# Kernel optimization log

Measured on AMD Instinct MI355X. Metric: run time of the kernel, lower is better.

Reference implementation:

```python
import jax, jax.numpy as jnp
import numpy as np

DIM = 512
NUM_HEADS = 16
WS = 8  # window_size
N = WS * WS
B = 1024


def get_relative_index(h, w):
    coords_h = np.arange(h)[:, None].repeat(w, axis=1)
    coords_w = np.arange(w)[None, :].repeat(h, axis=0)
    coords = np.stack([coords_h, coords_w], axis=-1).reshape(-1, 2)  # [N,2]
    rel = coords[:, None, :] - coords[None, :, :]
    rel = rel + np.array([h - 1, w - 1])
    rel[:, :, 0] *= 2 * w - 1
    return rel.sum(-1).astype(np.int32)  # [N,N]


def setup_inputs() -> dict:
    key = jax.random.key(0)
    ks = jax.random.split(key, 6)
    table_size = (2 * WS - 1) * (2 * WS - 1)  # 225
    return {
        "x": jax.random.normal(ks[0], (B, N, DIM), dtype=jnp.float32),
        "qkv_weight": jax.random.normal(ks[1], (3 * DIM, DIM), dtype=jnp.float32) * 0.02,
        "qkv_bias": jax.random.normal(ks[2], (3 * DIM,), dtype=jnp.float32) * 0.02,
        "proj_weight": jax.random.normal(ks[3], (DIM, DIM), dtype=jnp.float32) * 0.02,
        "proj_bias": jax.random.normal(ks[4], (DIM,), dtype=jnp.float32) * 0.02,
        "relative_table": jax.random.normal(ks[5], (table_size, 2 * NUM_HEADS), dtype=jnp.float32) * 0.02,
        "relative_index": jnp.asarray(get_relative_index(WS, WS)),
    }


def reference(x, qkv_weight, qkv_bias, proj_weight, proj_bias, relative_table, relative_index):
    B_, n, C = x.shape
    H = NUM_HEADS
    hd = C // H
    scale = hd ** -0.5
    # qkv projection: [B,N,3C] -> [3,B,H,N,hd]
    qkv = (x @ qkv_weight.T + qkv_bias).reshape(B_, n, 3, H, hd).transpose(2, 0, 3, 1, 4)
    q, k, v = qkv[0], qkv[1], qkv[2]
    attn = jnp.einsum("bhnd,bhmd->bhnm", q * scale, k)  # [B,H,N,N]
    # learned relative-position bias + post-softmax scale
    params = relative_table[relative_index.reshape(-1)].reshape(n, n, 2 * H)
    params = params.transpose(2, 0, 1)  # [2H,N,N]
    rel_bias, rel_scale = params[:H], params[H:]
    attn = jax.nn.softmax(attn + rel_bias[None], axis=-1)
    attn = attn * rel_scale[None]
    out = jnp.einsum("bhnm,bhmd->bhnd", attn, v)
    out = out.transpose(0, 2, 1, 3).reshape(B_, n, C)
    return out @ proj_weight.T + proj_bias
```

## Files before the change

kernel.cpp:

```cpp
#include <hip/hip_runtime.h>

typedef unsigned short u16;
typedef unsigned int   u32;
typedef __attribute__((ext_vector_type(8))) short bf16x8;
typedef __attribute__((ext_vector_type(4))) float f32x4;

#define SCALE 0.17677669529663687f

__device__ __forceinline__ u16 f2bf(float f){
  u32 x = __float_as_uint(f);
  x += 0x7fffu + ((x >> 16) & 1u);
  return (u16)(x >> 16);
}
__device__ __forceinline__ float bf2f(u16 u){
  return __uint_as_float(((u32)u) << 16);
}


__global__ void prep_kernel(const float* __restrict__ qkvw, const float* __restrict__ projw,
                            const float* __restrict__ table, const int* __restrict__ relidx,
                            u16* __restrict__ qkvw_b, u16* __restrict__ projw_b,
                            u16* __restrict__ biasT, u16* __restrict__ scaleT){
  int i = blockIdx.x * 256 + threadIdx.x;
  if (i < 786432) {
    qkvw_b[i] = f2bf(qkvw[i]);
  } else if (i < 1048576) {
    int j = i - 786432; projw_b[j] = f2bf(projw[j]);
  } else if (i < 1114112) {
    int j = i - 1048576; int h = j >> 12, rc = j & 4095;
    int idx = relidx[rc];
    biasT [h*4096 + rc] = f2bf(table[idx*32 + h]);
    scaleT[h*4096 + rc] = f2bf(table[idx*32 + 16 + h]);
  }
}

__global__ void xconv_kernel(const float* __restrict__ x, u16* __restrict__ xb){
  size_t i = (size_t)blockIdx.x * 256 + threadIdx.x;
  const float4* xp = (const float4*)x;
  float4 a = xp[2*i], b = xp[2*i+1];
  union { u16 u[8]; uint4 v; } o;
  o.u[0]=f2bf(a.x); o.u[1]=f2bf(a.y); o.u[2]=f2bf(a.z); o.u[3]=f2bf(a.w);
  o.u[4]=f2bf(b.x); o.u[5]=f2bf(b.y); o.u[6]=f2bf(b.z); o.u[7]=f2bf(b.w);
  *(uint4*)(xb + 8*i) = o.v;
}

template<int EPI>
__global__ __launch_bounds__(512, 4) void gemm_kernel(
    const u16* __restrict__ A, const u16* __restrict__ W,
    const float* __restrict__ bias, void* __restrict__ outp, const int NT)
{
  __shared__ u16 lds[3][12288];
  const int tid = threadIdx.x, lane = tid & 63;
  const int wid = tid >> 6, wave_base = tid & ~63;

  const int cpx = gridDim.x >> 3;
  const int bid = (blockIdx.x & 7) * cpx + (blockIdx.x >> 3);
  const int mt = bid / NT, nt = bid % NT;
  const size_t m0 = (size_t)mt * 128;
  const int n0 = nt * 256;
  const int wm = wid >> 2, wn = wid & 3;

  const f32x4 z = {0.f, 0.f, 0.f, 0.f};
  f32x4 acc[4][4];
#pragma unroll
  for (int i = 0; i < 4; i++)
#pragma unroll
    for (int j = 0; j < 4; j++) acc[i][j] = z;

  auto stage = [&](int ch){
    const int slot = ch % 3;
    const int kb = ch * 32;
    {
      const int row = tid >> 2, sl = tid & 3;
      const int lsl = sl ^ ((row >> 1) & 3);
      const u16* ga = A + (m0 + row)*512 + kb + lsl*8;
      u16* la = &lds[slot][(size_t)wave_base*8];
      __builtin_amdgcn_global_load_lds((const __attribute__((address_space(1))) u32*)ga,
                                       (__attribute__((address_space(3))) u32*)la, 16, 0, 0);
    }
#pragma unroll
    for (int c = 0; c < 2; ++c){
      const int t = c*512 + tid;
      const int col = t >> 2, sl = t & 3;
      const int lsl = sl ^ ((col >> 1) & 3);
      const u16* gb = W + (size_t)(n0 + col)*512 + kb + lsl*8;
      u16* lb = &lds[slot][4096 + (size_t)(c*512 + wave_base)*8];
      __builtin_amdgcn_global_load_lds((const __attribute__((address_space(1))) u32*)gb,
                                       (__attribute__((address_space(3))) u32*)lb, 16, 0, 0);
    }
  };

  stage(0);
  stage(1);
  asm volatile("s_waitcnt vmcnt(3)" ::: "memory");
  __builtin_amdgcn_s_barrier();

  const int lq = lane & 15, lk = lane >> 4;
#pragma unroll
  for (int ch = 0; ch < 16; ++ch){
    const int slot = ch % 3;
    if (ch + 2 < 16) stage(ch + 2);
    const u16* As = &lds[slot][0];
    const u16* Bs = &lds[slot][4096];
    bf16x8 af[4], bfr[4];
#pragma unroll
    for (int i = 0; i < 4; ++i){
      const int row = wm*64 + i*16 + lq;
      af[i]  = *(const bf16x8*)&As[row*32 + (lk ^ ((row >> 1) & 3))*8];
      const int col = wn*64 + i*16 + lq;
      bfr[i] = *(const bf16x8*)&Bs[col*32 + (lk ^ ((col >> 1) & 3))*8];
    }
    asm volatile("s_waitcnt lgkmcnt(0)" ::: "memory");
    __builtin_amdgcn_sched_barrier(0);
    __builtin_amdgcn_s_setprio(1);
#pragma unroll
    for (int i = 0; i < 4; ++i)
#pragma unroll
      for (int j = 0; j < 4; ++j)
        acc[i][j] = __builtin_amdgcn_mfma_f32_16x16x32_bf16(af[i], bfr[j], acc[i][j], 0, 0, 0);
    __builtin_amdgcn_s_setprio(0);
    if (ch <= 13)      { asm volatile("s_waitcnt vmcnt(3)" ::: "memory"); }
    else if (ch == 14) { asm volatile("s_waitcnt vmcnt(0)" ::: "memory"); }
    if (ch < 15) __builtin_amdgcn_s_barrier();
  }

  const int lr = (lane >> 4) << 2;
  const int lc = lane & 15;
  if (EPI == 0){
    u16* o = (u16*)outp;
    float bv[4], sc[4];
#pragma unroll
    for (int nf = 0; nf < 4; ++nf){
      const int col = n0 + wn*64 + nf*16 + lc;
      bv[nf] = bias[col];
      sc[nf] = (col < 512) ? SCALE : 1.f;
    }
#pragma unroll
    for (int mf = 0; mf < 4; ++mf){
#pragma unroll
      for (int r = 0; r < 4; ++r){
        const size_t row = m0 + wm*64 + mf*16 + lr + r;
#pragma unroll
        for (int nf = 0; nf < 4; ++nf){
          const int col = n0 + wn*64 + nf*16 + lc;
          o[row*1536 + col] = f2bf((acc[mf][nf][r] + bv[nf]) * sc[nf]);
        }
      }
    }
  } else {
    float* o = (float*)outp;
    float bv[4];
#pragma unroll
    for (int nf = 0; nf < 4; ++nf)
      bv[nf] = bias[n0 + wn*64 + nf*16 + lc];
#pragma unroll
    for (int mf = 0; mf < 4; ++mf){
#pragma unroll
      for (int r = 0; r < 4; ++r){
        const size_t row = m0 + wm*64 + mf*16 + lr + r;
#pragma unroll
        for (int nf = 0; nf < 4; ++nf){
          const int col = n0 + wn*64 + nf*16 + lc;
          o[row*512 + col] = acc[mf][nf][r] + bv[nf];
        }
      }
    }
  }
}

__global__ __launch_bounds__(256) void attn_kernel(
    const u16* __restrict__ qkv, const u16* __restrict__ biasT,
    const u16* __restrict__ scaleT, u16* __restrict__ attn_out)
{
  __shared__ u16 qs[64*40];
  __shared__ u16 ks[64*40];
  __shared__ u16 vs[64*40];
  __shared__ u16 Ps[64*72];
  const int tid = threadIdx.x, lane = tid & 63, wid = tid >> 6;
  const int bh = blockIdx.x, b = bh >> 4, h = bh & 15;
  const u16* base = qkv + (size_t)b * 64 * 1536 + h * 32;
  {
    const int row = tid >> 2, seg = (tid & 3) * 8;
    const size_t ro = (size_t)row * 1536 + seg;
    *(uint4*)&qs[row*40 + seg] = *(const uint4*)(base + ro);
    *(uint4*)&ks[row*40 + seg] = *(const uint4*)(base + ro + 512);
    *(uint4*)&vs[row*40 + seg] = *(const uint4*)(base + ro + 1024);
  }
  __syncthreads();

  const int wr0 = wid * 16;
  const int lg = lane >> 4, lc = lane & 15;
  const f32x4 z = {0.f, 0.f, 0.f, 0.f};

  bf16x8 qf = *(const bf16x8*)&qs[(wr0 + lc)*40 + lg*8];
  f32x4 s[4];
#pragma unroll
  for (int ct = 0; ct < 4; ++ct){
    bf16x8 kf = *(const bf16x8*)&ks[(ct*16 + lc)*40 + lg*8];
    s[ct] = __builtin_amdgcn_mfma_f32_16x16x32_bf16(qf, kf, z, 0, 0, 0);
  }

  const u16* bT = biasT + h*4096;
  const u16* sT = scaleT + h*4096;
#pragma unroll
  for (int r = 0; r < 4; ++r){
    const int row = wr0 + lg*4 + r;
    float vals[4]; float mx = -1e30f;
#pragma unroll
    for (int ct = 0; ct < 4; ++ct){
      vals[ct] = s[ct][r] + bf2f(bT[row*64 + ct*16 + lc]);
      mx = fmaxf(mx, vals[ct]);
    }
    mx = fmaxf(mx, __shfl_xor(mx, 1));
    mx = fmaxf(mx, __shfl_xor(mx, 2));
    mx = fmaxf(mx, __shfl_xor(mx, 4));
    mx = fmaxf(mx, __shfl_xor(mx, 8));
    float sm = 0.f;
#pragma unroll
    for (int ct = 0; ct < 4; ++ct){ vals[ct] = __expf(vals[ct] - mx); sm += vals[ct]; }
    sm += __shfl_xor(sm, 1);
    sm += __shfl_xor(sm, 2);
    sm += __shfl_xor(sm, 4);
    sm += __shfl_xor(sm, 8);
    const float inv = 1.f / sm;
#pragma unroll
    for (int ct = 0; ct < 4; ++ct){
      const int col = ct*16 + lc;
      Ps[row*72 + col] = f2bf(vals[ct] * inv * bf2f(sT[row*64 + col]));
    }
  }
  __syncthreads();

  f32x4 o[2] = {z, z};
#pragma unroll
  for (int kc = 0; kc < 2; ++kc){
    bf16x8 pf = *(const bf16x8*)&Ps[(wr0 + lc)*72 + kc*32 + lg*8];
#pragma unroll
    for (int c2 = 0; c2 < 2; ++c2){
      union { u16 u[8]; bf16x8 v; } vf;
#pragma unroll
      for (int e = 0; e < 8; ++e)
        vf.u[e] = vs[(kc*32 + lg*8 + e)*40 + c2*16 + lc];
      o[c2] = __builtin_amdgcn_mfma_f32_16x16x32_bf16(pf, vf.v, o[c2], 0, 0, 0);
    }
  }

#pragma unroll
  for (int c2 = 0; c2 < 2; ++c2){
#pragma unroll
    for (int r = 0; r < 4; ++r){
      const int n = wr0 + lg*4 + r;
      attn_out[((size_t)b*64 + n)*512 + h*32 + c2*16 + lc] = f2bf(o[c2][r]);
    }
  }
}

extern "C" void kernel_launch(void* const* d_in, const int* in_sizes, int n_in,
                              void* d_out, int out_size, void* d_ws, size_t ws_size,
                              hipStream_t stream)
{
  const float* x      = (const float*)d_in[0];
  const float* qkvw   = (const float*)d_in[1];
  const float* qkvb   = (const float*)d_in[2];
  const float* projw  = (const float*)d_in[3];
  const float* projb  = (const float*)d_in[4];
  const float* table  = (const float*)d_in[5];
  const int*   relidx = (const int*)d_in[6];
  char* ws = (char*)d_ws;

  u16* qkvw_b = (u16*)(ws + 0);
  u16* projw_b= (u16*)(ws + 1572864);
  u16* biasT  = (u16*)(ws + 2097152);
  u16* scaleT = (u16*)(ws + 2228224);
  u16* qkvws  = (u16*)(ws + 2359296);
  u16* xb     = (u16*)(ws + 203685888);
  u16* attn_o = xb;

  if (ws_size < 270794752ull) return;

  prep_kernel<<<dim3(4352), dim3(256), 0, stream>>>(qkvw, projw, table, relidx,
                                                    qkvw_b, projw_b, biasT, scaleT);
  xconv_kernel<<<dim3(16384), dim3(256), 0, stream>>>(x, xb);
  gemm_kernel<0><<<dim3(3072), dim3(512), 0, stream>>>(xb, qkvw_b, qkvb, (void*)qkvws, 6);
  attn_kernel<<<dim3(16384), dim3(256), 0, stream>>>(qkvws, biasT, scaleT, attn_o);
  gemm_kernel<1><<<dim3(1024), dim3(512), 0, stream>>>(attn_o, projw_b, projb, d_out, 2);
}
```

Before: 296.4 us.

## Enlarge GEMM tile to 256x256 with K=64 double-buffered 8-phase pipeline

Both GEMMs now use 256x256 output tiles per block instead of 128x256, with each wave computing 128x64, and the grid sizes are halved to match. K is staged in chunks of 64, with two LDS buffers and an XOR swizzle over 8 slots. The main loop is split into eight phases per iteration, each phase interleaving half-tile global-to-LDS loads with MFMA work and reusing the B fragments across the two M halves. The aim is higher arithmetic intensity and fewer redundant global loads per FLOP. In exchange, register and LDS pressure rise (launch bounds drop to 2 blocks per CU), the block count falls, and many more barriers are added.

```diff
diff --git a/kernel.cpp b/kernel.cpp
--- a/kernel.cpp
+++ b/kernel.cpp
@@ -45,84 +45,109 @@
 }
 
 template<int EPI>
-__global__ __launch_bounds__(512, 4) void gemm_kernel(
+__global__ __launch_bounds__(512, 2) void gemm_kernel(
     const u16* __restrict__ A, const u16* __restrict__ W,
     const float* __restrict__ bias, void* __restrict__ outp, const int NT)
 {
-  __shared__ u16 lds[3][12288];
+  __shared__ u16 lds[2][32768];
   const int tid = threadIdx.x, lane = tid & 63;
   const int wid = tid >> 6, wave_base = tid & ~63;
 
   const int cpx = gridDim.x >> 3;
   const int bid = (blockIdx.x & 7) * cpx + (blockIdx.x >> 3);
   const int mt = bid / NT, nt = bid % NT;
-  const size_t m0 = (size_t)mt * 128;
+  const size_t m0 = (size_t)mt * 256;
   const int n0 = nt * 256;
   const int wm = wid >> 2, wn = wid & 3;
+  const int lq = lane & 15, lk = lane >> 4;
 
   const f32x4 z = {0.f, 0.f, 0.f, 0.f};
-  f32x4 acc[4][4];
-#pragma unroll
-  for (int i = 0; i < 4; i++)
+  f32x4 acc[8][4];
+#pragma unroll
+  for (int i = 0; i < 8; i++)
 #pragma unroll
     for (int j = 0; j < 4; j++) acc[i][j] = z;
 
-  auto stage = [&](int ch){
-    const int slot = ch % 3;
-    const int kb = ch * 32;
-    {
-      const int row = tid >> 2, sl = tid & 3;
-      const int lsl = sl ^ ((row >> 1) & 3);
-      const u16* ga = A + (m0 + row)*512 + kb + lsl*8;
-      u16* la = &lds[slot][(size_t)wave_base*8];
-      __builtin_amdgcn_global_load_lds((const __attribute__((address_space(1))) u32*)ga,
-                                       (__attribute__((address_space(3))) u32*)la, 16, 0, 0);
-    }
+  auto stage_half = [&](int t, int half){
+    const int buf = t & 1;
+    const int kb = t * 64;
+    const bool isB = half >= 2;
+    const int h01 = half & 1;
+    const u16* src = isB ? W : A;
+    const size_t r0 = isB ? (size_t)n0 : m0;
+    const int ldsoff = (isB ? 16384 : 0) + h01 * 8192;
 #pragma unroll
     for (int c = 0; c < 2; ++c){
-      const int t = c*512 + tid;
-      const int col = t >> 2, sl = t & 3;
-      const int lsl = sl ^ ((col >> 1) & 3);
-      const u16* gb = W + (size_t)(n0 + col)*512 + kb + lsl*8;
-      u16* lb = &lds[slot][4096 + (size_t)(c*512 + wave_base)*8];
-      __builtin_amdgcn_global_load_lds((const __attribute__((address_space(1))) u32*)gb,
-                                       (__attribute__((address_space(3))) u32*)lb, 16, 0, 0);
+      const int u = c*512 + tid;
+      const int tr = h01*128 + (u >> 3);
+      const int lsl = (u & 7) ^ (tr & 7);
+      const u16* g = src + (r0 + tr)*512 + kb + lsl*8;
+      u16* l = &lds[buf][ldsoff + (size_t)(c*512 + wave_base)*8];
+      __builtin_amdgcn_global_load_lds((const __attribute__((address_space(1))) u32*)g,
+                                       (__attribute__((address_space(3))) u32*)l, 16, 0, 0);
     }
   };
 
-  stage(0);
-  stage(1);
-  asm volatile("s_waitcnt vmcnt(3)" ::: "memory");
+  bf16x8 bfr[4];
+
+#define PHASE(BUF, MH, KH, READB, STAGE_STMT) do {                            \
+    bf16x8 af[4];                                                             \
+    _Pragma("unroll")                                                         \
+    for (int i_ = 0; i_ < 4; ++i_){                                           \
+      const int row_ = wm*128 + (MH)*64 + i_*16 + lq;                         \
+      af[i_] = *(const bf16x8*)&lds[BUF][row_*64 + (((KH)*4+lk)^(lq&7))*8];   \
+    }                                                                         \
+    if (READB){                                                               \
+      _Pragma("unroll")                                                       \
+      for (int j_ = 0; j_ < 4; ++j_){                                         \
+        const int col_ = wn*64 + j_*16 + lq;                                  \
+        bfr[j_] = *(const bf16x8*)&lds[BUF][16384 + col_*64 + (((KH)*4+lk)^(lq&7))*8]; \
+      }                                                                       \
+    }                                                                         \
+    STAGE_STMT;                                                               \
+    __builtin_amdgcn_s_barrier();                                             \
+    asm volatile("s_waitcnt lgkmcnt(0)" ::: "memory");                        \
+    __builtin_amdgcn_sched_barrier(0);                                        \
+    __builtin_amdgcn_s_setprio(1);                                            \
+    _Pragma("unroll")                                                         \
+    for (int i_ = 0; i_ < 4; ++i_)                                            \
+      _Pragma("unroll")                                                       \
+      for (int j_ = 0; j_ < 4; ++j_)                                          \
+        acc[(MH)*4+i_][j_] = __builtin_amdgcn_mfma_f32_16x16x32_bf16(         \
+            af[i_], bfr[j_], acc[(MH)*4+i_][j_], 0, 0, 0);                    \
+    __builtin_amdgcn_s_setprio(0);                                            \
+  } while(0)
+
+  stage_half(0, 0); stage_half(0, 1); stage_half(0, 2); stage_half(0, 3);
+  stage_half(1, 2);
+  asm volatile("s_waitcnt vmcnt(2)" ::: "memory");
   __builtin_amdgcn_s_barrier();
 
-  const int lq = lane & 15, lk = lane >> 4;
-#pragma unroll
-  for (int ch = 0; ch < 16; ++ch){
-    const int slot = ch % 3;
-    if (ch + 2 < 16) stage(ch + 2);
-    const u16* As = &lds[slot][0];
-    const u16* Bs = &lds[slot][4096];
-    bf16x8 af[4], bfr[4];
-#pragma unroll
-    for (int i = 0; i < 4; ++i){
-      const int row = wm*64 + i*16 + lq;
-      af[i]  = *(const bf16x8*)&As[row*32 + (lk ^ ((row >> 1) & 3))*8];
-      const int col = wn*64 + i*16 + lq;
-      bfr[i] = *(const bf16x8*)&Bs[col*32 + (lk ^ ((col >> 1) & 3))*8];
-    }
-    asm volatile("s_waitcnt lgkmcnt(0)" ::: "memory");
-    __builtin_amdgcn_sched_barrier(0);
-    __builtin_amdgcn_s_setprio(1);
-#pragma unroll
-    for (int i = 0; i < 4; ++i)
-#pragma unroll
-      for (int j = 0; j < 4; ++j)
-        acc[i][j] = __builtin_amdgcn_mfma_f32_16x16x32_bf16(af[i], bfr[j], acc[i][j], 0, 0, 0);
-    __builtin_amdgcn_s_setprio(0);
-    if (ch <= 13)      { asm volatile("s_waitcnt vmcnt(3)" ::: "memory"); }
-    else if (ch == 14) { asm volatile("s_waitcnt vmcnt(0)" ::: "memory"); }
-    if (ch < 15) __builtin_amdgcn_s_barrier();
-  }
+#pragma unroll
+  for (int it = 0; it < 4; ++it){
+    PHASE(0, 0, 0, true,  stage_half(2*it+1, 3));
+    __builtin_amdgcn_s_barrier();
+    PHASE(0, 1, 0, false, stage_half(2*it+1, 0));
+    __builtin_amdgcn_s_barrier();
+    PHASE(0, 0, 1, true,  stage_half(2*it+1, 1));
+    __builtin_amdgcn_s_barrier();
+    PHASE(0, 1, 1, false, if (it < 3) stage_half(2*it+2, 2));
+    if (it < 3) { asm volatile("s_waitcnt vmcnt(2)" ::: "memory"); }
+    else        { asm volatile("s_waitcnt vmcnt(0)" ::: "memory"); }
+    __builtin_amdgcn_s_barrier();
+    PHASE(1, 0, 0, true,  if (it < 3) stage_half(2*it+2, 3));
+    __builtin_amdgcn_s_barrier();
+    PHASE(1, 1, 0, false, if (it < 3) stage_half(2*it+2, 0));
+    __builtin_amdgcn_s_barrier();
+    PHASE(1, 0, 1, true,  if (it < 3) stage_half(2*it+2, 1));
+    __builtin_amdgcn_s_barrier();
+    PHASE(1, 1, 1, false, if (it < 3) stage_half(2*it+3, 2));
+    if (it < 3){
+      asm volatile("s_waitcnt vmcnt(2)" ::: "memory");
+      __builtin_amdgcn_s_barrier();
+    }
+  }
+#undef PHASE
 
   const int lr = (lane >> 4) << 2;
   const int lc = lane & 15;
@@ -136,10 +161,10 @@
       sc[nf] = (col < 512) ? SCALE : 1.f;
     }
 #pragma unroll
-    for (int mf = 0; mf < 4; ++mf){
+    for (int mf = 0; mf < 8; ++mf){
 #pragma unroll
       for (int r = 0; r < 4; ++r){
-        const size_t row = m0 + wm*64 + mf*16 + lr + r;
+        const size_t row = m0 + wm*128 + mf*16 + lr + r;
 #pragma unroll
         for (int nf = 0; nf < 4; ++nf){
           const int col = n0 + wn*64 + nf*16 + lc;
@@ -154,10 +179,10 @@
     for (int nf = 0; nf < 4; ++nf)
       bv[nf] = bias[n0 + wn*64 + nf*16 + lc];
 #pragma unroll
-    for (int mf = 0; mf < 4; ++mf){
+    for (int mf = 0; mf < 8; ++mf){
 #pragma unroll
       for (int r = 0; r < 4; ++r){
-        const size_t row = m0 + wm*64 + mf*16 + lr + r;
+        const size_t row = m0 + wm*128 + mf*16 + lr + r;
 #pragma unroll
         for (int nf = 0; nf < 4; ++nf){
           const int col = n0 + wn*64 + nf*16 + lc;
@@ -281,7 +306,7 @@
   prep_kernel<<<dim3(4352), dim3(256), 0, stream>>>(qkvw, projw, table, relidx,
                                                     qkvw_b, projw_b, biasT, scaleT);
   xconv_kernel<<<dim3(16384), dim3(256), 0, stream>>>(x, xb);
-  gemm_kernel<0><<<dim3(3072), dim3(512), 0, stream>>>(xb, qkvw_b, qkvb, (void*)qkvws, 6);
+  gemm_kernel<0><<<dim3(1536), dim3(512), 0, stream>>>(xb, qkvw_b, qkvb, (void*)qkvws, 6);
   attn_kernel<<<dim3(16384), dim3(256), 0, stream>>>(qkvws, biasT, scaleT, attn_o);
-  gemm_kernel<1><<<dim3(1024), dim3(512), 0, stream>>>(attn_o, projw_b, projb, d_out, 2);
-}
+  gemm_kernel<1><<<dim3(512), dim3(512), 0, stream>>>(attn_o, projw_b, projb, d_out, 2);
+}
```

Result: faster. 287.6 us (-3.0%).

## Fuse fp32-to-bf16 conversion of x into the QKV GEMM A-tile load

Applied to the files above, without the earlier changes.

Drops the separate x conversion kernel. The QKV GEMM now loads fp32 x directly into registers, converts to bf16 and writes the swizzled LDS tile, pipelined two chunks ahead alongside the async global_load_lds for weights. This avoids writing and re-reading a 64 MB bf16 copy of x plus one kernel launch. The cost is that x is re-read once for each of the 6 N-tiles, in fp32 at twice the bytes, and each iteration adds register pressure and conversion ALU work.

```diff
diff --git a/kernel.cpp b/kernel.cpp
--- a/kernel.cpp
+++ b/kernel.cpp
@@ -34,20 +34,9 @@
   }
 }
 
-__global__ void xconv_kernel(const float* __restrict__ x, u16* __restrict__ xb){
-  size_t i = (size_t)blockIdx.x * 256 + threadIdx.x;
-  const float4* xp = (const float4*)x;
-  float4 a = xp[2*i], b = xp[2*i+1];
-  union { u16 u[8]; uint4 v; } o;
-  o.u[0]=f2bf(a.x); o.u[1]=f2bf(a.y); o.u[2]=f2bf(a.z); o.u[3]=f2bf(a.w);
-  o.u[4]=f2bf(b.x); o.u[5]=f2bf(b.y); o.u[6]=f2bf(b.z); o.u[7]=f2bf(b.w);
-  *(uint4*)(xb + 8*i) = o.v;
-}
-
-template<int EPI>
-__global__ __launch_bounds__(512, 4) void gemm_kernel(
-    const u16* __restrict__ A, const u16* __restrict__ W,
-    const float* __restrict__ bias, void* __restrict__ outp, const int NT)
+__global__ __launch_bounds__(512, 4) void gemm_qkv_kernel(
+    const float* __restrict__ X, const u16* __restrict__ W,
+    const float* __restrict__ bias, u16* __restrict__ outp)
 {
   __shared__ u16 lds[3][12288];
   const int tid = threadIdx.x, lane = tid & 63;
@@ -55,7 +44,129 @@
 
   const int cpx = gridDim.x >> 3;
   const int bid = (blockIdx.x & 7) * cpx + (blockIdx.x >> 3);
-  const int mt = bid / NT, nt = bid % NT;
+  const int mt = bid / 6, nt = bid % 6;
+  const size_t m0 = (size_t)mt * 128;
+  const int n0 = nt * 256;
+  const int wm = wid >> 2, wn = wid & 3;
+
+  const f32x4 z = {0.f, 0.f, 0.f, 0.f};
+  f32x4 acc[4][4];
+#pragma unroll
+  for (int i = 0; i < 4; i++)
+#pragma unroll
+    for (int j = 0; j < 4; j++) acc[i][j] = z;
+
+  const int arow = tid >> 2, asl = tid & 3;
+  const float* ag = X + (m0 + arow)*512 + asl*8;
+  const int awoff = arow*32 + (asl ^ ((arow >> 1) & 3))*8;
+
+  float4 arg[2][2];
+
+  auto stageB = [&](int ch){
+    const int slot = ch % 3;
+    const int kb = ch * 32;
+#pragma unroll
+    for (int c = 0; c < 2; ++c){
+      const int t = c*512 + tid;
+      const int col = t >> 2, sl = t & 3;
+      const int lsl = sl ^ ((col >> 1) & 3);
+      const u16* gb = W + (size_t)(n0 + col)*512 + kb + lsl*8;
+      u16* lb = &lds[slot][4096 + (size_t)(c*512 + wave_base)*8];
+      __builtin_amdgcn_global_load_lds((const __attribute__((address_space(1))) u32*)gb,
+                                       (__attribute__((address_space(3))) u32*)lb, 16, 0, 0);
+    }
+  };
+  auto issueA = [&](int ch, int s){
+    arg[s][0] = *(const float4*)(ag + ch*32);
+    arg[s][1] = *(const float4*)(ag + ch*32 + 4);
+  };
+  auto writeA = [&](int ch, int s){
+    union { u16 u[8]; bf16x8 v; } o;
+    const float* f = (const float*)&arg[s][0];
+#pragma unroll
+    for (int e = 0; e < 8; ++e) o.u[e] = f2bf(f[e]);
+    *(bf16x8*)&lds[ch % 3][awoff] = o.v;
+  };
+
+  issueA(0, 0);
+  issueA(1, 1);
+  stageB(0); stageB(1);
+  asm volatile("s_waitcnt vmcnt(6)" ::: "memory");
+  writeA(0, 0);
+  asm volatile("s_waitcnt vmcnt(2)" ::: "memory");
+  asm volatile("s_waitcnt lgkmcnt(0)" ::: "memory");
+  __builtin_amdgcn_s_barrier();
+
+  const int lq = lane & 15, lk = lane >> 4;
+#pragma unroll
+  for (int ch = 0; ch < 16; ++ch){
+    const int slot = ch % 3;
+    if (ch + 2 < 16){ issueA(ch + 2, ch & 1); stageB(ch + 2); }
+    const u16* As = &lds[slot][0];
+    const u16* Bs = &lds[slot][4096];
+    bf16x8 af[4], bfr[4];
+#pragma unroll
+    for (int i = 0; i < 4; ++i){
+      const int row = wm*64 + i*16 + lq;
+      af[i]  = *(const bf16x8*)&As[row*32 + (lk ^ ((row >> 1) & 3))*8];
+      const int col = wn*64 + i*16 + lq;
+      bfr[i] = *(const bf16x8*)&Bs[col*32 + (lk ^ ((col >> 1) & 3))*8];
+    }
+    asm volatile("s_waitcnt lgkmcnt(0)" ::: "memory");
+    __builtin_amdgcn_sched_barrier(0);
+    __builtin_amdgcn_s_setprio(1);
+#pragma unroll
+    for (int i = 0; i < 4; ++i)
+#pragma unroll
+      for (int j = 0; j < 4; ++j)
+        acc[i][j] = __builtin_amdgcn_mfma_f32_16x16x32_bf16(af[i], bfr[j], acc[i][j], 0, 0, 0);
+    __builtin_amdgcn_s_setprio(0);
+    if (ch < 15){
+      if (ch + 2 < 16) { asm volatile("s_waitcnt vmcnt(6)" ::: "memory"); }
+      else             { asm volatile("s_waitcnt vmcnt(2)" ::: "memory"); }
+      writeA(ch + 1, (ch + 1) & 1);
+      if (ch + 2 < 16) { asm volatile("s_waitcnt vmcnt(4)" ::: "memory"); }
+      else             { asm volatile("s_waitcnt vmcnt(0)" ::: "memory"); }
+      asm volatile("s_waitcnt lgkmcnt(0)" ::: "memory");
+      __builtin_amdgcn_s_barrier();
+    }
+  }
+
+  const int lr = (lane >> 4) << 2;
+  const int lc = lane & 15;
+  u16* o = outp;
+  float bv[4], sc[4];
+#pragma unroll
+  for (int nf = 0; nf < 4; ++nf){
+    const int col = n0 + wn*64 + nf*16 + lc;
+    bv[nf] = bias[col];
+    sc[nf] = (col < 512) ? SCALE : 1.f;
+  }
+#pragma unroll
+  for (int mf = 0; mf < 4; ++mf){
+#pragma unroll
+    for (int r = 0; r < 4; ++r){
+      const size_t row = m0 + wm*64 + mf*16 + lr + r;
+#pragma unroll
+      for (int nf = 0; nf < 4; ++nf){
+        const int col = n0 + wn*64 + nf*16 + lc;
+        o[row*1536 + col] = f2bf((acc[mf][nf][r] + bv[nf]) * sc[nf]);
+      }
+    }
+  }
+}
+
+__global__ __launch_bounds__(512, 4) void gemm_proj_kernel(
+    const u16* __restrict__ A, const u16* __restrict__ W,
+    const float* __restrict__ bias, float* __restrict__ outp)
+{
+  __shared__ u16 lds[3][12288];
+  const int tid = threadIdx.x, lane = tid & 63;
+  const int wid = tid >> 6, wave_base = tid & ~63;
+
+  const int cpx = gridDim.x >> 3;
+  const int bid = (blockIdx.x & 7) * cpx + (blockIdx.x >> 3);
+  const int mt = bid >> 1, nt = bid & 1;
   const size_t m0 = (size_t)mt * 128;
   const int n0 = nt * 256;
   const int wm = wid >> 2, wn = wid & 3;
@@ -126,43 +237,19 @@
 
   const int lr = (lane >> 4) << 2;
   const int lc = lane & 15;
-  if (EPI == 0){
-    u16* o = (u16*)outp;
-    float bv[4], sc[4];
-#pragma unroll
-    for (int nf = 0; nf < 4; ++nf){
-      const int col = n0 + wn*64 + nf*16 + lc;
-      bv[nf] = bias[col];
-      sc[nf] = (col < 512) ? SCALE : 1.f;
-    }
-#pragma unroll
-    for (int mf = 0; mf < 4; ++mf){
-#pragma unroll
-      for (int r = 0; r < 4; ++r){
-        const size_t row = m0 + wm*64 + mf*16 + lr + r;
-#pragma unroll
-        for (int nf = 0; nf < 4; ++nf){
-          const int col = n0 + wn*64 + nf*16 + lc;
-          o[row*1536 + col] = f2bf((acc[mf][nf][r] + bv[nf]) * sc[nf]);
-        }
-      }
-    }
-  } else {
-    float* o = (float*)outp;
-    float bv[4];
-#pragma unroll
-    for (int nf = 0; nf < 4; ++nf)
-      bv[nf] = bias[n0 + wn*64 + nf*16 + lc];
-#pragma unroll
-    for (int mf = 0; mf < 4; ++mf){
-#pragma unroll
-      for (int r = 0; r < 4; ++r){
-        const size_t row = m0 + wm*64 + mf*16 + lr + r;
-#pragma unroll
-        for (int nf = 0; nf < 4; ++nf){
-          const int col = n0 + wn*64 + nf*16 + lc;
-          o[row*512 + col] = acc[mf][nf][r] + bv[nf];
-        }
+  float bv[4];
+#pragma unroll
+  for (int nf = 0; nf < 4; ++nf)
+    bv[nf] = bias[n0 + wn*64 + nf*16 + lc];
+#pragma unroll
+  for (int mf = 0; mf < 4; ++mf){
+#pragma unroll
+    for (int r = 0; r < 4; ++r){
+      const size_t row = m0 + wm*64 + mf*16 + lr + r;
+#pragma unroll
+      for (int nf = 0; nf < 4; ++nf){
+        const int col = n0 + wn*64 + nf*16 + lc;
+        outp[row*512 + col] = acc[mf][nf][r] + bv[nf];
       }
     }
   }
@@ -273,15 +360,13 @@
   u16* biasT  = (u16*)(ws + 2097152);
   u16* scaleT = (u16*)(ws + 2228224);
   u16* qkvws  = (u16*)(ws + 2359296);
-  u16* xb     = (u16*)(ws + 203685888);
-  u16* attn_o = xb;
+  u16* attn_o = (u16*)(ws + 203685888);
 
   if (ws_size < 270794752ull) return;
 
   prep_kernel<<<dim3(4352), dim3(256), 0, stream>>>(qkvw, projw, table, relidx,
                                                     qkvw_b, projw_b, biasT, scaleT);
-  xconv_kernel<<<dim3(16384), dim3(256), 0, stream>>>(x, xb);
-  gemm_kernel<0><<<dim3(3072), dim3(512), 0, stream>>>(xb, qkvw_b, qkvb, (void*)qkvws, 6);
+  gemm_qkv_kernel<<<dim3(3072), dim3(512), 0, stream>>>(x, qkvw_b, qkvb, qkvws);
   attn_kernel<<<dim3(16384), dim3(256), 0, stream>>>(qkvws, biasT, scaleT, attn_o);
-  gemm_kernel<1><<<dim3(1024), dim3(512), 0, stream>>>(attn_o, projw_b, projb, d_out, 2);
-}
+  gemm_proj_kernel<<<dim3(1024), dim3(512), 0, stream>>>(attn_o, projw_b, projb, (float*)d_out);
+}
```

Measured after the change: 321.5 us. 1.08x slower.
